# Optimization experiments

Hardware: AMD Instinct MI355X
Metric: run time of the kernel (lower is better)

Reference implementation:

```python
import jax, jax.numpy as jnp
import numpy as np

N = 16384   # 32 graphs x 512 nodes
E_RAND = 500000
H, C, D, F, L = 4, 64, 256, 1024, 4  # heads, head_dim, model dim, ffn dim, layers


def setup_inputs() -> dict:
    key = jax.random.key(0)
    ks = jax.random.split(key, 8)
    ei = jax.random.randint(ks[0], (2, E_RAND), 0, N)
    loops = jnp.arange(N)
    edge_index = jnp.concatenate([ei, jnp.stack([loops, loops])], axis=1)  # add_self_loops
    s = 0.05
    return dict(
        hf=jax.random.normal(ks[1], (N, D), dtype=jnp.float32),
        hs=jax.random.normal(ks[2], (N, D), dtype=jnp.float32),
        edge_index=edge_index,
        Wgat=jax.random.normal(ks[3], (2, L, D, D), dtype=jnp.float32) * s,
        att_src=jax.random.normal(ks[4], (2, L, H, C), dtype=jnp.float32) * s,
        att_dst=jax.random.normal(ks[5], (2, L, H, C), dtype=jnp.float32) * s,
        bias_gat=jnp.zeros((2, L, D), dtype=jnp.float32),
        W1=jax.random.normal(ks[6], (2, L, D, F), dtype=jnp.float32) * s,
        b1=jnp.zeros((2, L, F), dtype=jnp.float32),
        W2=jax.random.normal(ks[7], (2, L, F, D), dtype=jnp.float32) * s,
        b2=jnp.zeros((2, L, D), dtype=jnp.float32),
        g1=jnp.ones((2, L, D), dtype=jnp.float32),
        bt1=jnp.zeros((2, L, D), dtype=jnp.float32),
        g2=jnp.ones((2, L, D), dtype=jnp.float32),
        bt2=jnp.zeros((2, L, D), dtype=jnp.float32),
    )


def _ln(x, g, b):
    m = jnp.mean(x, -1, keepdims=True)
    v = jnp.var(x, -1, keepdims=True)
    return (x - m) * jax.lax.rsqrt(v + 1e-5) * g + b


def _gat_encoder_layer(x, src, dst, Wg, asr, ads, bg, W1, b1, W2, b2, g1, bt1, g2, bt2):
    # GATConv (PyG semantics): linear proj, per-edge attention, segment softmax over dst
    h = (x @ Wg).reshape(N, H, C)                       # [N,H,C]
    a_s = (h * asr).sum(-1)                             # [N,H]
    a_d = (h * ads).sum(-1)                             # [N,H]
    e = jax.nn.leaky_relu(a_s[src] + a_d[dst], 0.2)     # [E,H]
    m = jax.ops.segment_max(e, dst, num_segments=N)
    ex = jnp.exp(e - m[dst])
    den = jax.ops.segment_sum(ex, dst, num_segments=N)
    alpha = ex / jnp.maximum(den[dst], 1e-16)           # [E,H]
    agg = jax.ops.segment_sum(h[src] * alpha[:, :, None], dst, num_segments=N)
    out = agg.reshape(N, H * C) + bg                    # concat heads + bias
    # residual + norm1 (dropout=0.0)
    x1 = _ln(out + x, g1, bt1)
    # FFN + residual + norm2
    f = jax.nn.relu(x1 @ W1 + b1) @ W2 + b2
    return _ln(f + x1, g2, bt2)


def reference(hf, hs, edge_index, Wgat, att_src, att_dst, bias_gat, W1, b1, W2, b2, g1, bt1, g2, bt2):
    src, dst = edge_index[0], edge_index[1]
    for i in range(L):
        hf_new = _gat_encoder_layer(hf + hs, src, dst, Wgat[0, i], att_src[0, i], att_dst[0, i],
                                    bias_gat[0, i], W1[0, i], b1[0, i], W2[0, i], b2[0, i],
                                    g1[0, i], bt1[0, i], g2[0, i], bt2[0, i])
        hs = _gat_encoder_layer(hs, src, dst, Wgat[1, i], att_src[1, i], att_dst[1, i],
                                bias_gat[1, i], W1[1, i], b1[1, i], W2[1, i], b2[1, i],
                                g1[1, i], bt1[1, i], g2[1, i], bt2[1, i])
        hf = hf_new
    return (hf, hs)
```

## Files before the change

kernel.cpp:

```cpp
#include <hip/hip_runtime.h>

#define Nn 16384
#define Dm 256
#define Ff 1024

typedef __attribute__((ext_vector_type(8))) short bf16x8;
typedef __attribute__((ext_vector_type(4))) float f32x4;

typedef const __attribute__((address_space(1))) unsigned int glb_u32;
typedef __attribute__((address_space(3))) unsigned int lds_u32;

__device__ __forceinline__ void async_copy16(const void* g, void* l) {
  __builtin_amdgcn_global_load_lds((glb_u32*)g, (lds_u32*)l, 16, 0, 0);
}

__device__ __forceinline__ unsigned short f2bf(float f) {
  union { float f; unsigned u; } v; v.f = f;
  return (unsigned short)((v.u + 0x7FFFu + ((v.u >> 16) & 1u)) >> 16);
}

__device__ __forceinline__ float bf2f(unsigned short u) {
  union { unsigned u; float f; } v; v.u = ((unsigned)u) << 16;
  return v.f;
}

__device__ __forceinline__ float sel4(float4 v, int h) {
  float r = v.x;
  r = (h == 1) ? v.y : r;
  r = (h == 2) ? v.z : r;
  r = (h == 3) ? v.w : r;
  return r;
}

__global__ __launch_bounds__(256) void wconvt_kernel(const float* __restrict__ w,
                                                     unsigned short* __restrict__ wt,
                                                     int K, int J) {
  __shared__ unsigned short t[64][65];
  int b = blockIdx.z;
  int j0 = blockIdx.x * 64, k0 = blockIdx.y * 64;
  int tj = threadIdx.x & 63, q = threadIdx.x >> 6;
  const float* wb = w + (size_t)b * K * J;
#pragma unroll
  for (int r = 0; r < 16; ++r) {
    int k = r * 4 + q;
    t[k][tj] = f2bf(wb[(size_t)(k0 + k) * J + j0 + tj]);
  }
  __syncthreads();
  unsigned short* wtb = wt + (size_t)b * K * J;
#pragma unroll
  for (int r = 0; r < 16; ++r) {
    int j = r * 4 + q;
    wtb[(size_t)(j0 + j) * K + k0 + tj] = t[tj][j];
  }
}

__global__ void count_kernel(const int* __restrict__ dst, int E, int* __restrict__ cnt) {
  for (int e = blockIdx.x * blockDim.x + threadIdx.x; e < E; e += gridDim.x * blockDim.x)
    atomicAdd(&cnt[dst[e]], 1);
}

__global__ __launch_bounds__(256) void scan1_kernel(const int* __restrict__ cnt,
                                                    int* __restrict__ part,
                                                    int* __restrict__ bsum) {
  __shared__ int sd[256];
  int b = blockIdx.x, tid = threadIdx.x;
  int v = cnt[b * 256 + tid];
  sd[tid] = v;
  __syncthreads();
  for (int offt = 1; offt < 256; offt <<= 1) {
    int t = (tid >= offt) ? sd[tid - offt] : 0;
    __syncthreads();
    sd[tid] += t;
    __syncthreads();
  }
  part[b * 256 + tid] = sd[tid] - v;
  if (tid == 255) bsum[b] = sd[255];
}

__global__ __launch_bounds__(64) void scan2_kernel(const int* __restrict__ bsum,
                                                   int* __restrict__ bbase,
                                                   int* __restrict__ rowptr) {
  __shared__ int sd[64];
  int tid = threadIdx.x;
  int v = bsum[tid];
  sd[tid] = v;
  __syncthreads();
  for (int offt = 1; offt < 64; offt <<= 1) {
    int t = (tid >= offt) ? sd[tid - offt] : 0;
    __syncthreads();
    sd[tid] += t;
    __syncthreads();
  }
  bbase[tid] = sd[tid] - v;
  if (tid == 63) rowptr[Nn] = sd[63];
}

__global__ __launch_bounds__(256) void scan3_kernel(const int* __restrict__ part,
                                                    const int* __restrict__ bbase,
                                                    int* __restrict__ rowptr,
                                                    int* __restrict__ cursor) {
  int b = blockIdx.x, tid = threadIdx.x;
  int v = part[b * 256 + tid] + bbase[b];
  rowptr[b * 256 + tid] = v;
  cursor[b * 256 + tid] = v;
}

__global__ void fill_kernel(const int* __restrict__ src, const int* __restrict__ dst, int E,
                            int* __restrict__ cursor, int* __restrict__ csrc) {
  for (int e = blockIdx.x * blockDim.x + threadIdx.x; e < E; e += gridDim.x * blockDim.x) {
    int pos = atomicAdd(&cursor[dst[e]], 1);
    csrc[pos] = src[e];
  }
}

__global__ void prep_kernel(const float* __restrict__ hf, const float* __restrict__ hs,
                            unsigned short* __restrict__ x01b, int total) {
  const size_t ZS = (size_t)Nn * Dm;
  for (int i = blockIdx.x * blockDim.x + threadIdx.x; i < total; i += gridDim.x * blockDim.x) {
    float a = hf[i], b = hs[i];
    x01b[i] = f2bf(a + b);
    x01b[ZS + i] = f2bf(b);
  }
}

__global__ __launch_bounds__(256, 3) void proj_kernel(
    const unsigned short* __restrict__ xib, const unsigned short* __restrict__ Wgt_l,
    unsigned short* __restrict__ hbuf2, const float* __restrict__ asr_l,
    const float* __restrict__ ads_l, float* __restrict__ a_s2, float* __restrict__ a_d2) {
  __shared__ __align__(16) unsigned short sA[128 * 64];
  __shared__ __align__(16) unsigned short sB[64 * 64];
  const int K = 256;
  const size_t ZS = (size_t)Nn * Dm;
  int tid = threadIdx.x;
  int wave = tid >> 6, lane = tid & 63;
  int l16 = lane & 15, lhi = lane >> 4;
  int brow = blockIdx.x, bcol = blockIdx.y, z = blockIdx.z;
  int wm = wave >> 1, wn = wave & 1;

  const unsigned short* Ab = xib + z * ZS + (size_t)brow * 128 * K;
  const unsigned short* Bb = Wgt_l + (size_t)z * 4 * 65536 + (size_t)bcol * 64 * K;
  int lrow = lane >> 3, lk = (lane & 7) * 8;

  f32x4 acc[4][2] = {};

  for (int k0 = 0; k0 < K; k0 += 64) {
#pragma unroll
    for (int r = 0; r < 4; ++r) {
      int rb = r * 32 + wave * 8;
      async_copy16(Ab + (size_t)(rb + lrow) * K + k0 + lk, &sA[rb * 64]);
      if (r < 2)
        async_copy16(Bb + (size_t)(rb + lrow) * K + k0 + lk, &sB[rb * 64]);
    }
    __syncthreads();
#pragma unroll
    for (int kk = 0; kk < 2; ++kk) {
      bf16x8 af[4], bfr[2];
#pragma unroll
      for (int mi = 0; mi < 4; ++mi)
        af[mi] = *(const bf16x8*)&sA[(wm * 64 + mi * 16 + l16) * 64 + kk * 32 + lhi * 8];
#pragma unroll
      for (int ni = 0; ni < 2; ++ni)
        bfr[ni] = *(const bf16x8*)&sB[(wn * 32 + ni * 16 + l16) * 64 + kk * 32 + lhi * 8];
#pragma unroll
      for (int mi = 0; mi < 4; ++mi)
#pragma unroll
        for (int ni = 0; ni < 2; ++ni)
          acc[mi][ni] = __builtin_amdgcn_mfma_f32_16x16x32_bf16(af[mi], bfr[ni], acc[mi][ni], 0, 0, 0);
    }
    __syncthreads();
  }

  unsigned short* hb = hbuf2 + z * ZS;
  const float* asr_p = asr_l + z * 1024 + bcol * 64;
  const float* ads_p = ads_l + z * 1024 + bcol * 64;
  float as0 = asr_p[wn * 32 + l16],      ad0 = ads_p[wn * 32 + l16];
  float as1 = asr_p[wn * 32 + 16 + l16], ad1 = ads_p[wn * 32 + 16 + l16];
  float* sredS = (float*)sA;
  float* sredD = (float*)sA + 256;

#pragma unroll
  for (int mi = 0; mi < 4; ++mi) {
#pragma unroll
    for (int j = 0; j < 4; ++j) {
      int r = brow * 128 + wm * 64 + mi * 16 + lhi * 4 + j;
      float v0 = acc[mi][0][j], v1 = acc[mi][1][j];
      hb[(size_t)r * 256 + bcol * 64 + wn * 32 + l16] = f2bf(v0);
      hb[(size_t)r * 256 + bcol * 64 + wn * 32 + 16 + l16] = f2bf(v1);
      float ps = v0 * as0 + v1 * as1;
      float pd = v0 * ad0 + v1 * ad1;
#pragma unroll
      for (int off = 1; off < 16; off <<= 1) {
        ps += __shfl_xor(ps, off);
        pd += __shfl_xor(pd, off);
      }
      if (l16 == 0) {
        int rl = mi * 16 + lhi * 4 + j;
        sredS[wm * 128 + wn * 64 + rl] = ps;
        sredD[wm * 128 + wn * 64 + rl] = pd;
      }
    }
  }
  __syncthreads();
  if (tid < 128) {
    int w = tid >> 6, rl = tid & 63;
    float s = sredS[w * 128 + rl] + sredS[w * 128 + 64 + rl];
    float d = sredD[w * 128 + rl] + sredD[w * 128 + 64 + rl];
    int row = brow * 128 + tid;
    a_s2[(size_t)z * Nn * 4 + row * 4 + bcol] = s;
    a_d2[(size_t)z * Nn * 4 + row * 4 + bcol] = d;
  }
}

__global__ __launch_bounds__(256, 3) void ffn1_kernel(
    const unsigned short* __restrict__ A2, const unsigned short* __restrict__ Bt_l,
    unsigned short* __restrict__ out2, const float* __restrict__ b1_l) {
  const int K = 256, Ncol = Ff;
  const size_t ZS = (size_t)Nn * Dm;
  __shared__ __align__(16) unsigned short sA[128 * 64];
  __shared__ __align__(16) unsigned short sB[128 * 64];
  int tid = threadIdx.x, wave = tid >> 6, lane = tid & 63;
  int l16 = lane & 15, lhi = lane >> 4;
  int brow = blockIdx.x, bcol = blockIdx.y, z = blockIdx.z;
  int wm = wave >> 1, wn = wave & 1;

  const unsigned short* Ab = A2 + z * ZS + (size_t)brow * 128 * K;
  const unsigned short* Bb = Bt_l + (size_t)z * 4 * Ff * 256 + (size_t)bcol * 128 * K;
  int lrow = lane >> 3, lk = (lane & 7) * 8;

  f32x4 acc[4][4] = {};

  for (int k0 = 0; k0 < K; k0 += 64) {
#pragma unroll
    for (int r = 0; r < 4; ++r) {
      int rb = r * 32 + wave * 8;
      async_copy16(Ab + (size_t)(rb + lrow) * K + k0 + lk, &sA[rb * 64]);
      async_copy16(Bb + (size_t)(rb + lrow) * K + k0 + lk, &sB[rb * 64]);
    }
    __syncthreads();
#pragma unroll
    for (int kk = 0; kk < 2; ++kk) {
      bf16x8 af[4], bfr[4];
#pragma unroll
      for (int mi = 0; mi < 4; ++mi)
        af[mi] = *(const bf16x8*)&sA[(wm * 64 + mi * 16 + l16) * 64 + kk * 32 + lhi * 8];
#pragma unroll
      for (int ni = 0; ni < 4; ++ni)
        bfr[ni] = *(const bf16x8*)&sB[(wn * 64 + ni * 16 + l16) * 64 + kk * 32 + lhi * 8];
#pragma unroll
      for (int mi = 0; mi < 4; ++mi)
#pragma unroll
        for (int ni = 0; ni < 4; ++ni)
          acc[mi][ni] = __builtin_amdgcn_mfma_f32_16x16x32_bf16(af[mi], bfr[ni], acc[mi][ni], 0, 0, 0);
    }
    __syncthreads();
  }

  unsigned short* outB = out2 + (size_t)z * Nn * Ff;
  const float* bias = b1_l + z * 4096;
#pragma unroll
  for (int mi = 0; mi < 4; ++mi) {
#pragma unroll
    for (int ni = 0; ni < 4; ++ni) {
#pragma unroll
      for (int j = 0; j < 4; ++j) {
        int r = brow * 128 + wm * 64 + mi * 16 + lhi * 4 + j;
        int c = bcol * 128 + wn * 64 + ni * 16 + l16;
        float v = acc[mi][ni][j] + bias[c];
        v = v > 0.f ? v : 0.f;
        outB[(size_t)r * Ncol + c] = f2bf(v);
      }
    }
  }
}

__global__ __launch_bounds__(256, 3) void ffn2_kernel(
    const unsigned short* __restrict__ A2, const unsigned short* __restrict__ Bt_l,
    unsigned short* __restrict__ out2, const float* __restrict__ b2_l,
    const unsigned short* __restrict__ resid2) {
  const int K = Ff, Ncol = 256;
  const size_t ZS = (size_t)Nn * Dm;
  __shared__ __align__(16) unsigned short sA[128 * 64];
  __shared__ __align__(16) unsigned short sB[64 * 64];
  int tid = threadIdx.x, wave = tid >> 6, lane = tid & 63;
  int l16 = lane & 15, lhi = lane >> 4;
  int brow = blockIdx.x, bcol = blockIdx.y, z = blockIdx.z;
  int wm = wave >> 1, wn = wave & 1;

  const unsigned short* Ab = A2 + (size_t)z * Nn * Ff + (size_t)brow * 128 * K;
  const unsigned short* Bb = Bt_l + (size_t)z * 4 * Ff * 256 + (size_t)bcol * 64 * K;
  int lrow = lane >> 3, lk = (lane & 7) * 8;

  f32x4 acc[4][2] = {};

  for (int k0 = 0; k0 < K; k0 += 64) {
#pragma unroll
    for (int r = 0; r < 4; ++r) {
      int rb = r * 32 + wave * 8;
      async_copy16(Ab + (size_t)(rb + lrow) * K + k0 + lk, &sA[rb * 64]);
      if (r < 2)
        async_copy16(Bb + (size_t)(rb + lrow) * K + k0 + lk, &sB[rb * 64]);
    }
    __syncthreads();
#pragma unroll
    for (int kk = 0; kk < 2; ++kk) {
      bf16x8 af[4], bfr[2];
#pragma unroll
      for (int mi = 0; mi < 4; ++mi)
        af[mi] = *(const bf16x8*)&sA[(wm * 64 + mi * 16 + l16) * 64 + kk * 32 + lhi * 8];
#pragma unroll
      for (int ni = 0; ni < 2; ++ni)
        bfr[ni] = *(const bf16x8*)&sB[(wn * 32 + ni * 16 + l16) * 64 + kk * 32 + lhi * 8];
#pragma unroll
      for (int mi = 0; mi < 4; ++mi)
#pragma unroll
        for (int ni = 0; ni < 2; ++ni)
          acc[mi][ni] = __builtin_amdgcn_mfma_f32_16x16x32_bf16(af[mi], bfr[ni], acc[mi][ni], 0, 0, 0);
    }
    __syncthreads();
  }

  unsigned short* outB = out2 + z * ZS;
  const float* bias = b2_l + z * 1024;
  const unsigned short* resid = resid2 + z * ZS;
#pragma unroll
  for (int mi = 0; mi < 4; ++mi) {
#pragma unroll
    for (int ni = 0; ni < 2; ++ni) {
#pragma unroll
      for (int j = 0; j < 4; ++j) {
        int r = brow * 128 + wm * 64 + mi * 16 + lhi * 4 + j;
        int c = bcol * 64 + wn * 32 + ni * 16 + l16;
        float v = acc[mi][ni][j] + bias[c] + bf2f(resid[(size_t)r * Ncol + c]);
        outB[(size_t)r * Ncol + c] = f2bf(v);
      }
    }
  }
}

__global__ __launch_bounds__(256) void agg_kernel(
    const unsigned short* __restrict__ hbuf2, const float* __restrict__ a_s2,
    const float* __restrict__ a_d2,
    const int* __restrict__ rowptr, const int* __restrict__ csrc,
    const float* __restrict__ bias_l, const unsigned short* __restrict__ x01b,
    const float* __restrict__ g1_l, const float* __restrict__ bt1_l,
    unsigned short* __restrict__ x1b2, int z) {
  __shared__ float sw[4][320];
  __shared__ int ssrc[4][64];
  const size_t ZS = (size_t)Nn * Dm;
  const unsigned short* hb = hbuf2 + z * ZS;
  const float* a_s = a_s2 + (size_t)z * Nn * 4;
  const float* a_d = a_d2 + (size_t)z * Nn * 4;
  const float* bias = bias_l + z * 1024;
  const unsigned short* xres = x01b + z * ZS;
  const float* g1 = g1_l + z * 1024;
  const float* bt1 = bt1_l + z * 1024;
  unsigned short* x1b = x1b2 + z * ZS;

  int wave = threadIdx.x >> 6, lane = threadIdx.x & 63;
  int n = blockIdx.x * 4 + wave;
  int l32 = lane & 31;
  int par = lane >> 5;
  int hch = l32 >> 3;
  int c0 = l32 * 8;
  int beg = rowptr[n], end = rowptr[n + 1];
  float4 adv = *(const float4*)&a_d[n * 4];
  const float NI = -__builtin_inff();
  float acc[8] = {};
  float den = 0.f;

  if (end - beg <= 64) {
    int cnt = end - beg;
    float4 ev = {NI, NI, NI, NI};
    if (lane < cnt) {
      int s = csrc[beg + lane];
      ssrc[wave][lane] = s;
      float4 as = *(const float4*)&a_s[s * 4];
      float e0 = as.x + adv.x; ev.x = e0 > 0.f ? e0 : 0.2f * e0;
      float e1 = as.y + adv.y; ev.y = e1 > 0.f ? e1 : 0.2f * e1;
      float e2 = as.z + adv.z; ev.z = e2 > 0.f ? e2 : 0.2f * e2;
      float e3 = as.w + adv.w; ev.w = e3 > 0.f ? e3 : 0.2f * e3;
    }
    float4 mv = ev;
#pragma unroll
    for (int off = 32; off; off >>= 1) {
      mv.x = fmaxf(mv.x, __shfl_xor(mv.x, off));
      mv.y = fmaxf(mv.y, __shfl_xor(mv.y, off));
      mv.z = fmaxf(mv.z, __shfl_xor(mv.z, off));
      mv.w = fmaxf(mv.w, __shfl_xor(mv.w, off));
    }
    if (lane < cnt) {
      float* swl = &sw[wave][lane * 5];
      swl[0] = __expf(ev.x - mv.x);
      swl[1] = __expf(ev.y - mv.y);
      swl[2] = __expf(ev.z - mv.z);
      swl[3] = __expf(ev.w - mv.w);
    }
    __builtin_amdgcn_wave_barrier();
    for (int i = par; i < cnt; i += 2) {
      float w = sw[wave][i * 5 + hch];
      int s_i = ssrc[wave][i];
      bf16x8 hv = *(const bf16x8*)(hb + (size_t)s_i * 256 + c0);
#pragma unroll
      for (int j = 0; j < 8; ++j)
        acc[j] = fmaf(bf2f((unsigned short)hv[j]), w, acc[j]);
      den += w;
    }
  } else {
    float4 m4 = {NI, NI, NI, NI};
    for (int base = beg; base < end; base += 64) {
      int cnt = min(64, end - base);
      float4 ev = {NI, NI, NI, NI};
      if (lane < cnt) {
        int s = csrc[base + lane];
        ssrc[wave][lane] = s;
        float4 as = *(const float4*)&a_s[s * 4];
        float e0 = as.x + adv.x; ev.x = e0 > 0.f ? e0 : 0.2f * e0;
        float e1 = as.y + adv.y; ev.y = e1 > 0.f ? e1 : 0.2f * e1;
        float e2 = as.z + adv.z; ev.z = e2 > 0.f ? e2 : 0.2f * e2;
        float e3 = as.w + adv.w; ev.w = e3 > 0.f ? e3 : 0.2f * e3;
      }
      float4 mv = ev;
#pragma unroll
      for (int off = 32; off; off >>= 1) {
        mv.x = fmaxf(mv.x, __shfl_xor(mv.x, off));
        mv.y = fmaxf(mv.y, __shfl_xor(mv.y, off));
        mv.z = fmaxf(mv.z, __shfl_xor(mv.z, off));
        mv.w = fmaxf(mv.w, __shfl_xor(mv.w, off));
      }
      float4 m4n;
      m4n.x = fmaxf(m4.x, mv.x); m4n.y = fmaxf(m4.y, mv.y);
      m4n.z = fmaxf(m4.z, mv.z); m4n.w = fmaxf(m4.w, mv.w);
      float rm = __expf(sel4(m4, hch) - sel4(m4n, hch));
#pragma unroll
      for (int j = 0; j < 8; ++j) acc[j] *= rm;
      den *= rm;
      if (lane < cnt) {
        float* swl = &sw[wave][lane * 5];
        swl[0] = __expf(ev.x - m4n.x);
        swl[1] = __expf(ev.y - m4n.y);
        swl[2] = __expf(ev.z - m4n.z);
        swl[3] = __expf(ev.w - m4n.w);
      }
      m4 = m4n;
      __builtin_amdgcn_wave_barrier();
      for (int i = par; i < cnt; i += 2) {
        float w = sw[wave][i * 5 + hch];
        int s_i = ssrc[wave][i];
        bf16x8 hv = *(const bf16x8*)(hb + (size_t)s_i * 256 + c0);
#pragma unroll
        for (int j = 0; j < 8; ++j)
          acc[j] = fmaf(bf2f((unsigned short)hv[j]), w, acc[j]);
        den += w;
      }
      __builtin_amdgcn_wave_barrier();
    }
  }

#pragma unroll
  for (int j = 0; j < 8; ++j) acc[j] += __shfl_xor(acc[j], 32);
  den += __shfl_xor(den, 32);

  float invden = 1.f / fmaxf(den, 1e-16f);
  bf16x8 rv = *(const bf16x8*)(xres + (size_t)n * 256 + c0);
  float outv[8];
  float s1 = 0.f, s2 = 0.f;
#pragma unroll
  for (int j = 0; j < 8; ++j) {
    float v = acc[j] * invden + bias[c0 + j] + bf2f((unsigned short)rv[j]);
    outv[j] = v;
    s1 += v;
    s2 += v * v;
  }
#pragma unroll
  for (int off = 16; off; off >>= 1) {
    s1 += __shfl_xor(s1, off);
    s2 += __shfl_xor(s2, off);
  }
  float mean = s1 * (1.f / 256.f);
  float var = s2 * (1.f / 256.f) - mean * mean;
  float rst = rsqrtf(var + 1e-5f);
  if (par == 0) {
    unsigned short yb[8];
#pragma unroll
    for (int j = 0; j < 8; ++j)
      yb[j] = f2bf((outv[j] - mean) * rst * g1[c0 + j] + bt1[c0 + j]);
    *(bf16x8*)&x1b[(size_t)n * 256 + c0] = *(bf16x8*)yb;
  }
}

template <int PREP>
__global__ __launch_bounds__(256) void ln2_kernel(const unsigned short* __restrict__ tb2,
                                                  const float* __restrict__ g2_l,
                                                  const float* __restrict__ bt2_l,
                                                  float* __restrict__ out_hf,
                                                  float* __restrict__ out_hs,
                                                  unsigned short* __restrict__ x01b) {
  const size_t ZS = (size_t)Nn * Dm;
  int wave = threadIdx.x >> 6, lane = threadIdx.x & 63;
  int n = blockIdx.x * 4 + wave;
  int c0 = lane * 4;
  size_t idx = (size_t)n * 256 + c0;
  ushort4 u0 = *(const ushort4*)&tb2[idx];
  ushort4 u1 = *(const ushort4*)&tb2[ZS + idx];
  float v0[4] = {bf2f(u0.x), bf2f(u0.y), bf2f(u0.z), bf2f(u0.w)};
  float v1[4] = {bf2f(u1.x), bf2f(u1.y), bf2f(u1.z), bf2f(u1.w)};
  float a0 = 0.f, b0 = 0.f, a1 = 0.f, b1 = 0.f;
#pragma unroll
  for (int j = 0; j < 4; ++j) {
    a0 += v0[j]; b0 += v0[j] * v0[j];
    a1 += v1[j]; b1 += v1[j] * v1[j];
  }
#pragma unroll
  for (int off = 32; off; off >>= 1) {
    a0 += __shfl_xor(a0, off);
    b0 += __shfl_xor(b0, off);
    a1 += __shfl_xor(a1, off);
    b1 += __shfl_xor(b1, off);
  }
  float m0 = a0 * (1.f / 256.f), m1 = a1 * (1.f / 256.f);
  float r0 = rsqrtf(b0 * (1.f / 256.f) - m0 * m0 + 1e-5f);
  float r1 = rsqrtf(b1 * (1.f / 256.f) - m1 * m1 + 1e-5f);
  float4 y0, y1;
  unsigned short p0[4], p1[4];
#pragma unroll
  for (int j = 0; j < 4; ++j) {
    float yf = (v0[j] - m0) * r0 * g2_l[c0 + j] + bt2_l[c0 + j];
    float ys = (v1[j] - m1) * r1 * g2_l[1024 + c0 + j] + bt2_l[1024 + c0 + j];
    ((float*)&y0)[j] = yf;
    ((float*)&y1)[j] = ys;
    if (PREP) { p0[j] = f2bf(yf + ys); p1[j] = f2bf(ys); }
  }
  *(float4*)&out_hf[idx] = y0;
  *(float4*)&out_hs[idx] = y1;
  if (PREP) {
    *(ushort4*)&x01b[idx] = *(ushort4*)p0;
    *(ushort4*)&x01b[ZS + idx] = *(ushort4*)p1;
  }
}

extern "C" void kernel_launch(void* const* d_in, const int* in_sizes, int n_in,
                              void* d_out, int out_size, void* d_ws, size_t ws_size,
                              hipStream_t stream) {
  const float* hf_in = (const float*)d_in[0];
  const float* hs_in = (const float*)d_in[1];
  const int* ei = (const int*)d_in[2];
  const int E = in_sizes[2] / 2;
  const float* Wgat = (const float*)d_in[3];
  const float* att_src = (const float*)d_in[4];
  const float* att_dst = (const float*)d_in[5];
  const float* bias_gat = (const float*)d_in[6];
  const float* W1 = (const float*)d_in[7];
  const float* b1 = (const float*)d_in[8];
  const float* W2 = (const float*)d_in[9];
  const float* b2 = (const float*)d_in[10];
  const float* g1 = (const float*)d_in[11];
  const float* bt1 = (const float*)d_in[12];
  const float* g2 = (const float*)d_in[13];
  const float* bt2 = (const float*)d_in[14];
  const int* src = ei;
  const int* dst = ei + E;
  const size_t ZS = (size_t)Nn * Dm;

  char* wsp = (char*)d_ws;
  size_t off = 0;
  auto carve = [&](size_t bytes) -> void* {
    void* p = wsp + off;
    off += (bytes + 255) & ~(size_t)255;
    return p;
  };
  unsigned short* Wgt  = (unsigned short*)carve((size_t)8 * 256 * 256 * 2);
  unsigned short* W1t  = (unsigned short*)carve((size_t)8 * 256 * 1024 * 2);
  unsigned short* W2t  = (unsigned short*)carve((size_t)8 * 1024 * 256 * 2);
  int* cnt      = (int*)carve((size_t)Nn * 4);
  int* rowptr   = (int*)carve((size_t)(Nn + 1) * 4);
  int* cursor   = (int*)carve((size_t)Nn * 4);
  int* part     = (int*)carve((size_t)Nn * 4);
  int* bsum     = (int*)carve((size_t)64 * 4);
  int* bbase    = (int*)carve((size_t)64 * 4);
  int* csrc     = (int*)carve((size_t)E * 4);
  unsigned short* x01b = (unsigned short*)carve(2 * ZS * 2);
  unsigned short* hbuf2 = (unsigned short*)carve(2 * ZS * 2);
  float* a_s2   = (float*)carve((size_t)2 * Nn * 4 * 4);
  float* a_d2   = (float*)carve((size_t)2 * Nn * 4 * 4);
  unsigned short* x1b2 = (unsigned short*)carve(2 * ZS * 2);
  unsigned short* tb2  = (unsigned short*)carve(2 * ZS * 2);
  unsigned short* f_b2 = (unsigned short*)carve((size_t)2 * Nn * Ff * 2);
  if (off > ws_size) return;

  wconvt_kernel<<<dim3(4, 4, 8), 256, 0, stream>>>(Wgat, Wgt, 256, 256);
  wconvt_kernel<<<dim3(16, 4, 8), 256, 0, stream>>>(W1, W1t, 256, 1024);
  wconvt_kernel<<<dim3(4, 16, 8), 256, 0, stream>>>(W2, W2t, 1024, 256);
  hipMemsetAsync(cnt, 0, (size_t)Nn * 4, stream);
  count_kernel<<<1024, 256, 0, stream>>>(dst, E, cnt);
  scan1_kernel<<<64, 256, 0, stream>>>(cnt, part, bsum);
  scan2_kernel<<<1, 64, 0, stream>>>(bsum, bbase, rowptr);
  scan3_kernel<<<64, 256, 0, stream>>>(part, bbase, rowptr, cursor);
  fill_kernel<<<1024, 256, 0, stream>>>(src, dst, E, cursor, csrc);

  float* out_hf = (float*)d_out;
  float* out_hs = out_hf + ZS;

  prep_kernel<<<2048, 256, 0, stream>>>(hf_in, hs_in, x01b, Nn * Dm);

  for (int l = 0; l < 4; ++l) {
    proj_kernel<<<dim3(128, 4, 2), 256, 0, stream>>>(
        x01b, Wgt + (size_t)l * 65536, hbuf2,
        att_src + l * 256, att_dst + l * 256, a_s2, a_d2);
    agg_kernel<<<Nn / 4, 256, 0, stream>>>(
        hbuf2, a_s2, a_d2, rowptr, csrc,
        bias_gat + l * 256, x01b, g1 + l * 256, bt1 + l * 256, x1b2, 0);
    agg_kernel<<<Nn / 4, 256, 0, stream>>>(
        hbuf2, a_s2, a_d2, rowptr, csrc,
        bias_gat + l * 256, x01b, g1 + l * 256, bt1 + l * 256, x1b2, 1);
    ffn1_kernel<<<dim3(128, 8, 2), 256, 0, stream>>>(
        x1b2, W1t + (size_t)l * 256 * 1024, f_b2, b1 + l * 1024);
    ffn2_kernel<<<dim3(128, 4, 2), 256, 0, stream>>>(
        f_b2, W2t + (size_t)l * 1024 * 256, tb2, b2 + l * 256, x1b2);
    if (l < 3) {
      ln2_kernel<1><<<Nn / 4, 256, 0, stream>>>(tb2, g2 + l * 256, bt2 + l * 256,
                                                out_hf, out_hs, x01b);
    } else {
      ln2_kernel<0><<<Nn / 4, 256, 0, stream>>>(tb2, g2 + l * 256, bt2 + l * 256,
                                                out_hf, out_hs, x01b);
    }
  }
}
```

Before: 681.2 us.

## Double-buffer GEMM LDS tiles, unify FFN GEMMs, merge agg launches

Adds double-buffered shared-memory staging to the projection and FFN GEMMs, so the async global-to-LDS copy of the next K tile is issued before the MFMA work on the current tile. The two FFN kernels are merged into one templated 128x128-tile GEMM, which gives the second FFN GEMM a wider N tile (fewer column blocks, more reuse of the A operand). The two per-stream aggregation launches become a single 2D grid. The doubled LDS footprint lowers launch_bounds occupancy from 3 to 2 blocks per CU. This trades latency hiding through occupancy for latency hiding through prefetch.

```diff
diff --git a/kernel.cpp b/kernel.cpp
--- a/kernel.cpp
+++ b/kernel.cpp
@@ -123,12 +123,12 @@
   }
 }
 
-__global__ __launch_bounds__(256, 3) void proj_kernel(
+__global__ __launch_bounds__(256, 2) void proj_kernel(
     const unsigned short* __restrict__ xib, const unsigned short* __restrict__ Wgt_l,
     unsigned short* __restrict__ hbuf2, const float* __restrict__ asr_l,
     const float* __restrict__ ads_l, float* __restrict__ a_s2, float* __restrict__ a_d2) {
-  __shared__ __align__(16) unsigned short sA[128 * 64];
-  __shared__ __align__(16) unsigned short sB[64 * 64];
+  __shared__ __align__(16) unsigned short sA[2][128 * 64];
+  __shared__ __align__(16) unsigned short sB[2][64 * 64];
   const int K = 256;
   const size_t ZS = (size_t)Nn * Dm;
   int tid = threadIdx.x;
@@ -143,24 +143,31 @@
 
   f32x4 acc[4][2] = {};
 
-  for (int k0 = 0; k0 < K; k0 += 64) {
+  auto stage = [&](int buf, int k0) {
 #pragma unroll
     for (int r = 0; r < 4; ++r) {
       int rb = r * 32 + wave * 8;
-      async_copy16(Ab + (size_t)(rb + lrow) * K + k0 + lk, &sA[rb * 64]);
+      async_copy16(Ab + (size_t)(rb + lrow) * K + k0 + lk, &sA[buf][rb * 64]);
       if (r < 2)
-        async_copy16(Bb + (size_t)(rb + lrow) * K + k0 + lk, &sB[rb * 64]);
-    }
-    __syncthreads();
+        async_copy16(Bb + (size_t)(rb + lrow) * K + k0 + lk, &sB[buf][rb * 64]);
+    }
+  };
+
+  stage(0, 0);
+  __syncthreads();
+  int cur = 0;
+#pragma unroll
+  for (int t = 0; t < 4; ++t) {
+    if (t < 3) stage(cur ^ 1, (t + 1) * 64);
 #pragma unroll
     for (int kk = 0; kk < 2; ++kk) {
       bf16x8 af[4], bfr[2];
 #pragma unroll
       for (int mi = 0; mi < 4; ++mi)
-        af[mi] = *(const bf16x8*)&sA[(wm * 64 + mi * 16 + l16) * 64 + kk * 32 + lhi * 8];
+        af[mi] = *(const bf16x8*)&sA[cur][(wm * 64 + mi * 16 + l16) * 64 + kk * 32 + lhi * 8];
 #pragma unroll
       for (int ni = 0; ni < 2; ++ni)
-        bfr[ni] = *(const bf16x8*)&sB[(wn * 32 + ni * 16 + l16) * 64 + kk * 32 + lhi * 8];
+        bfr[ni] = *(const bf16x8*)&sB[cur][(wn * 32 + ni * 16 + l16) * 64 + kk * 32 + lhi * 8];
 #pragma unroll
       for (int mi = 0; mi < 4; ++mi)
 #pragma unroll
@@ -168,6 +175,7 @@
           acc[mi][ni] = __builtin_amdgcn_mfma_f32_16x16x32_bf16(af[mi], bfr[ni], acc[mi][ni], 0, 0, 0);
     }
     __syncthreads();
+    cur ^= 1;
   }
 
   unsigned short* hb = hbuf2 + z * ZS;
@@ -211,41 +219,51 @@
   }
 }
 
-__global__ __launch_bounds__(256, 3) void ffn1_kernel(
-    const unsigned short* __restrict__ A2, const unsigned short* __restrict__ Bt_l,
-    unsigned short* __restrict__ out2, const float* __restrict__ b1_l) {
-  const int K = 256, Ncol = Ff;
-  const size_t ZS = (size_t)Nn * Dm;
-  __shared__ __align__(16) unsigned short sA[128 * 64];
-  __shared__ __align__(16) unsigned short sB[128 * 64];
+template <int EPI>
+__global__ __launch_bounds__(256, 2) void gemm128_kernel(
+    const unsigned short* __restrict__ A2, size_t aZ,
+    const unsigned short* __restrict__ Bt_l,
+    unsigned short* __restrict__ out2, size_t oZ,
+    const float* __restrict__ bias_l, int biasZ,
+    const unsigned short* __restrict__ resid2,
+    int K, int Ncol) {
+  __shared__ __align__(16) unsigned short sA[2][128 * 64];
+  __shared__ __align__(16) unsigned short sB[2][128 * 64];
   int tid = threadIdx.x, wave = tid >> 6, lane = tid & 63;
   int l16 = lane & 15, lhi = lane >> 4;
   int brow = blockIdx.x, bcol = blockIdx.y, z = blockIdx.z;
   int wm = wave >> 1, wn = wave & 1;
 
-  const unsigned short* Ab = A2 + z * ZS + (size_t)brow * 128 * K;
+  const unsigned short* Ab = A2 + z * aZ + (size_t)brow * 128 * K;
   const unsigned short* Bb = Bt_l + (size_t)z * 4 * Ff * 256 + (size_t)bcol * 128 * K;
   int lrow = lane >> 3, lk = (lane & 7) * 8;
 
   f32x4 acc[4][4] = {};
 
-  for (int k0 = 0; k0 < K; k0 += 64) {
+  auto stage = [&](int buf, int k0) {
 #pragma unroll
     for (int r = 0; r < 4; ++r) {
       int rb = r * 32 + wave * 8;
-      async_copy16(Ab + (size_t)(rb + lrow) * K + k0 + lk, &sA[rb * 64]);
-      async_copy16(Bb + (size_t)(rb + lrow) * K + k0 + lk, &sB[rb * 64]);
-    }
-    __syncthreads();
+      async_copy16(Ab + (size_t)(rb + lrow) * K + k0 + lk, &sA[buf][rb * 64]);
+      async_copy16(Bb + (size_t)(rb + lrow) * K + k0 + lk, &sB[buf][rb * 64]);
+    }
+  };
+
+  int NT = K >> 6;
+  stage(0, 0);
+  __syncthreads();
+  int cur = 0;
+  for (int t = 0; t < NT; ++t) {
+    if (t + 1 < NT) stage(cur ^ 1, (t + 1) * 64);
 #pragma unroll
     for (int kk = 0; kk < 2; ++kk) {
       bf16x8 af[4], bfr[4];
 #pragma unroll
       for (int mi = 0; mi < 4; ++mi)
-        af[mi] = *(const bf16x8*)&sA[(wm * 64 + mi * 16 + l16) * 64 + kk * 32 + lhi * 8];
+        af[mi] = *(const bf16x8*)&sA[cur][(wm * 64 + mi * 16 + l16) * 64 + kk * 32 + lhi * 8];
 #pragma unroll
       for (int ni = 0; ni < 4; ++ni)
-        bfr[ni] = *(const bf16x8*)&sB[(wn * 64 + ni * 16 + l16) * 64 + kk * 32 + lhi * 8];
+        bfr[ni] = *(const bf16x8*)&sB[cur][(wn * 64 + ni * 16 + l16) * 64 + kk * 32 + lhi * 8];
 #pragma unroll
       for (int mi = 0; mi < 4; ++mi)
 #pragma unroll
@@ -253,10 +271,12 @@
           acc[mi][ni] = __builtin_amdgcn_mfma_f32_16x16x32_bf16(af[mi], bfr[ni], acc[mi][ni], 0, 0, 0);
     }
     __syncthreads();
-  }
-
-  unsigned short* outB = out2 + (size_t)z * Nn * Ff;
-  const float* bias = b1_l + z * 4096;
+    cur ^= 1;
+  }
+
+  unsigned short* outB = out2 + z * oZ;
+  const float* bias = bias_l + z * biasZ;
+  const unsigned short* resid = (EPI == 2) ? resid2 + z * oZ : nullptr;
 #pragma unroll
   for (int mi = 0; mi < 4; ++mi) {
 #pragma unroll
@@ -266,71 +286,11 @@
         int r = brow * 128 + wm * 64 + mi * 16 + lhi * 4 + j;
         int c = bcol * 128 + wn * 64 + ni * 16 + l16;
         float v = acc[mi][ni][j] + bias[c];
-        v = v > 0.f ? v : 0.f;
-        outB[(size_t)r * Ncol + c] = f2bf(v);
-      }
-    }
-  }
-}
-
-__global__ __launch_bounds__(256, 3) void ffn2_kernel(
-    const unsigned short* __restrict__ A2, const unsigned short* __restrict__ Bt_l,
-    unsigned short* __restrict__ out2, const float* __restrict__ b2_l,
-    const unsigned short* __restrict__ resid2) {
-  const int K = Ff, Ncol = 256;
-  const size_t ZS = (size_t)Nn * Dm;
-  __shared__ __align__(16) unsigned short sA[128 * 64];
-  __shared__ __align__(16) unsigned short sB[64 * 64];
-  int tid = threadIdx.x, wave = tid >> 6, lane = tid & 63;
-  int l16 = lane & 15, lhi = lane >> 4;
-  int brow = blockIdx.x, bcol = blockIdx.y, z = blockIdx.z;
-  int wm = wave >> 1, wn = wave & 1;
-
-  const unsigned short* Ab = A2 + (size_t)z * Nn * Ff + (size_t)brow * 128 * K;
-  const unsigned short* Bb = Bt_l + (size_t)z * 4 * Ff * 256 + (size_t)bcol * 64 * K;
-  int lrow = lane >> 3, lk = (lane & 7) * 8;
-
-  f32x4 acc[4][2] = {};
-
-  for (int k0 = 0; k0 < K; k0 += 64) {
-#pragma unroll
-    for (int r = 0; r < 4; ++r) {
-      int rb = r * 32 + wave * 8;
-      async_copy16(Ab + (size_t)(rb + lrow) * K + k0 + lk, &sA[rb * 64]);
-      if (r < 2)
-        async_copy16(Bb + (size_t)(rb + lrow) * K + k0 + lk, &sB[rb * 64]);
-    }
-    __syncthreads();
-#pragma unroll
-    for (int kk = 0; kk < 2; ++kk) {
-      bf16x8 af[4], bfr[2];
-#pragma unroll
-      for (int mi = 0; mi < 4; ++mi)
-        af[mi] = *(const bf16x8*)&sA[(wm * 64 + mi * 16 + l16) * 64 + kk * 32 + lhi * 8];
-#pragma unroll
-      for (int ni = 0; ni < 2; ++ni)
-        bfr[ni] = *(const bf16x8*)&sB[(wn * 32 + ni * 16 + l16) * 64 + kk * 32 + lhi * 8];
-#pragma unroll
-      for (int mi = 0; mi < 4; ++mi)
-#pragma unroll
-        for (int ni = 0; ni < 2; ++ni)
-          acc[mi][ni] = __builtin_amdgcn_mfma_f32_16x16x32_bf16(af[mi], bfr[ni], acc[mi][ni], 0, 0, 0);
-    }
-    __syncthreads();
-  }
-
-  unsigned short* outB = out2 + z * ZS;
-  const float* bias = b2_l + z * 1024;
-  const unsigned short* resid = resid2 + z * ZS;
-#pragma unroll
-  for (int mi = 0; mi < 4; ++mi) {
-#pragma unroll
-    for (int ni = 0; ni < 2; ++ni) {
-#pragma unroll
-      for (int j = 0; j < 4; ++j) {
-        int r = brow * 128 + wm * 64 + mi * 16 + lhi * 4 + j;
-        int c = bcol * 64 + wn * 32 + ni * 16 + l16;
-        float v = acc[mi][ni][j] + bias[c] + bf2f(resid[(size_t)r * Ncol + c]);
+        if (EPI == 1) {
+          v = v > 0.f ? v : 0.f;
+        } else {
+          v += bf2f(resid[(size_t)r * Ncol + c]);
+        }
         outB[(size_t)r * Ncol + c] = f2bf(v);
       }
     }
@@ -343,10 +303,11 @@
     const int* __restrict__ rowptr, const int* __restrict__ csrc,
     const float* __restrict__ bias_l, const unsigned short* __restrict__ x01b,
     const float* __restrict__ g1_l, const float* __restrict__ bt1_l,
-    unsigned short* __restrict__ x1b2, int z) {
+    unsigned short* __restrict__ x1b2) {
   __shared__ float sw[4][320];
   __shared__ int ssrc[4][64];
   const size_t ZS = (size_t)Nn * Dm;
+  int z = blockIdx.y;
   const unsigned short* hb = hbuf2 + z * ZS;
   const float* a_s = a_s2 + (size_t)z * Nn * 4;
   const float* a_d = a_d2 + (size_t)z * Nn * 4;
@@ -606,16 +567,15 @@
     proj_kernel<<<dim3(128, 4, 2), 256, 0, stream>>>(
         x01b, Wgt + (size_t)l * 65536, hbuf2,
         att_src + l * 256, att_dst + l * 256, a_s2, a_d2);
-    agg_kernel<<<Nn / 4, 256, 0, stream>>>(
+    agg_kernel<<<dim3(Nn / 4, 2), 256, 0, stream>>>(
         hbuf2, a_s2, a_d2, rowptr, csrc,
-        bias_gat + l * 256, x01b, g1 + l * 256, bt1 + l * 256, x1b2, 0);
-    agg_kernel<<<Nn / 4, 256, 0, stream>>>(
-        hbuf2, a_s2, a_d2, rowptr, csrc,
-        bias_gat + l * 256, x01b, g1 + l * 256, bt1 + l * 256, x1b2, 1);
-    ffn1_kernel<<<dim3(128, 8, 2), 256, 0, stream>>>(
-        x1b2, W1t + (size_t)l * 256 * 1024, f_b2, b1 + l * 1024);
-    ffn2_kernel<<<dim3(128, 4, 2), 256, 0, stream>>>(
-        f_b2, W2t + (size_t)l * 1024 * 256, tb2, b2 + l * 256, x1b2);
+        bias_gat + l * 256, x01b, g1 + l * 256, bt1 + l * 256, x1b2);
+    gemm128_kernel<1><<<dim3(128, 8, 2), 256, 0, stream>>>(
+        x1b2, ZS, W1t + (size_t)l * 256 * 1024,
+        f_b2, (size_t)Nn * Ff, b1 + l * 1024, 4096, nullptr, 256, Ff);
+    gemm128_kernel<2><<<dim3(128, 2, 2), 256, 0, stream>>>(
+        f_b2, (size_t)Nn * Ff, W2t + (size_t)l * 1024 * 256,
+        tb2, ZS, b2 + l * 256, 1024, x1b2, 1024, 256);
     if (l < 3) {
       ln2_kernel<1><<<Nn / 4, 256, 0, stream>>>(tb2, g2 + l * 256, bt2 + l * 256,
                                                 out_hf, out_hs, x01b);
```

Result: slower. 701.7 us (+3.0%).
